# Kernel optimization log

Hardware: AMD Instinct MI355X
Metric: run time of the kernel (lower is better)

Reference implementation:

```python
import jax, jax.numpy as jnp
import numpy as np

NUM_ROUTES = 32 * 6 * 6  # 1152
NUM_CAPS = 10
IN_DIM = 8
OUT_DIM = 16
NUM_ITERS = 3

def _conv(x, w, stride):
    return jax.lax.conv_general_dilated(
        x, w, window_strides=(stride, stride), padding='VALID',
        dimension_numbers=('NCHW', 'OIHW', 'NCHW'))

def _squash(u):
    # squash over last axis, exactly as torch code (no eps)
    sn = (u ** 2).sum(-1, keepdims=True)
    return sn * u / ((1.0 + sn) * jnp.sqrt(sn))

def setup_inputs() -> dict:
    key = jax.random.key(0)
    ks = jax.random.split(key, 10)
    B = 512
    data = jax.random.normal(ks[0], (B, 1, 28, 28), dtype=jnp.float32)
    conv_w = jax.random.normal(ks[1], (256, 1, 9, 9), dtype=jnp.float32) * 0.05
    conv_b = jnp.zeros((256,), dtype=jnp.float32)
    # 8 primary-capsule convs stacked caps-major -> fused conv [8*32,256,9,9]
    pc_w = jax.random.normal(ks[2], (8 * 32, 256, 9, 9), dtype=jnp.float32) * 0.01
    pc_b = jnp.zeros((8 * 32,), dtype=jnp.float32)
    W = jax.random.normal(ks[3], (NUM_ROUTES, NUM_CAPS, OUT_DIM, IN_DIM), dtype=jnp.float32)
    enc_w1 = jax.random.normal(ks[4], (512, OUT_DIM * NUM_CAPS), dtype=jnp.float32) * 0.05
    enc_b1 = jnp.zeros((512,), dtype=jnp.float32)
    enc_w2 = jax.random.normal(ks[5], (9, 512), dtype=jnp.float32) * 0.05
    enc_b2 = jnp.zeros((9,), dtype=jnp.float32)
    return dict(data=data, conv_w=conv_w, conv_b=conv_b, pc_w=pc_w, pc_b=pc_b,
                W=W, enc_w1=enc_w1, enc_b1=enc_b1, enc_w2=enc_w2, enc_b2=enc_b2)

def reference(data, conv_w, conv_b, pc_w, pc_b, W, enc_w1, enc_b1, enc_w2, enc_b2):
    B = data.shape[0]
    # ConvLayer: conv + relu -> [B,256,20,20]
    x = jax.nn.relu(_conv(data, conv_w, 1) + conv_b[None, :, None, None])
    # PrimaryCaps: 8 stride-2 convs (fused, caps-major channels) -> [B,256,6,6]
    u = _conv(x, pc_w, 2) + pc_b[None, :, None, None]
    # torch: stack(dim=1) then view(B, num_routes, -1) == reshape caps-major flat
    u = u.reshape(B, NUM_ROUTES, IN_DIM)
    u = _squash(u)  # [B,R,8]
    # WaferCaps: u_hat[b,r,c,o] = sum_i W[r,c,o,i] * u[b,r,i]
    u_hat = jnp.einsum('rcoi,bri->brco', W, u)  # [B,R,C,O]
    b_ij = jnp.zeros((NUM_ROUTES, NUM_CAPS), dtype=u_hat.dtype)
    v = None
    for it in range(NUM_ITERS):
        c_ij = jax.nn.softmax(b_ij, axis=0)  # softmax over routes (dim=1 in torch)
        s = jnp.einsum('rc,brco->bco', c_ij, u_hat)  # [B,C,O]
        # original squashes [B,1,C,O,1] over last (size-1) dim -> elementwise
        s2 = s ** 2
        v = s2 * s / ((1.0 + s2) * jnp.sqrt(s2))  # = s*|s|/(1+s^2)
        if it < NUM_ITERS - 1:
            a = jnp.einsum('brco,bco->brc', u_hat, v)  # [B,R,C]
            b_ij = b_ij + a.mean(axis=0)
    # Encoder: flatten [B,C,O] row-major -> [B,160]
    flat = v.reshape(B, NUM_CAPS * OUT_DIM)
    h = jax.nn.relu(flat @ enc_w1.T + enc_b1)  # dropout is identity at eval
    out = jax.nn.sigmoid(h @ enc_w2.T + enc_b2)
    return out
```

## Files before the change

kernel.cpp:

```cpp
#include <hip/hip_runtime.h>
#include <hip/hip_bf16.h>
#include <stdint.h>


typedef __bf16 bf16_t;
typedef __bf16 bf16x4 __attribute__((ext_vector_type(4)));
typedef __bf16 bf16x8 __attribute__((ext_vector_type(8)));
typedef float f32x4 __attribute__((ext_vector_type(4)));
typedef int i32x4 __attribute__((ext_vector_type(4)));
typedef int i32x8 __attribute__((ext_vector_type(8)));

__device__ __forceinline__ void gload_lds16(const void* g, void* l) {
    __builtin_amdgcn_global_load_lds((const __attribute__((address_space(1))) void*)g,
                                     (__attribute__((address_space(3))) void*)l, 16, 0, 0);
}

#define MEMBAR() asm volatile("" ::: "memory")
#define HW_BARRIER() do { MEMBAR(); __builtin_amdgcn_s_barrier(); MEMBAR(); } while (0)

__device__ __forceinline__ uint8_t fp8b(float v) {
    return (uint8_t)(__builtin_amdgcn_cvt_pk_fp8_f32(v, 0.f, 0, false) & 0xFF);
}

__global__ void k_init_bij(float* bij) {
    int i = blockIdx.x * 256 + threadIdx.x;
    if (i < 1152 * 10) bij[i] = 0.f;
}

__global__ void k_w1t(const float* __restrict__ w1, float* __restrict__ w1t) {
    int i = blockIdx.x * 256 + threadIdx.x;
    int j = i / 160, k = i % 160;
    w1t[k * 512 + j] = w1[i];
}

__global__ void k_w1c(const float* __restrict__ cw, bf16_t* __restrict__ Bc1) {
    int idx = blockIdx.x * 256 + threadIdx.x;
    if (idx >= 26624) return;
    int oc = idx / 104, k = idx % 104;
    Bc1[idx] = (k < 81) ? (bf16_t)cw[oc * 81 + k] : (bf16_t)0.f;
}

__global__ __launch_bounds__(256) void k_w2t(const float* __restrict__ pcw,
                                             uint8_t* __restrict__ w2t8) {
    __shared__ uint16_t tmp16[10368];
    int oc = blockIdx.x, tid = threadIdx.x;
    const float* src = pcw + (size_t)oc * 20736;
    for (int q2 = tid; q2 < 10368; q2 += 256) {
        float a = src[q2 * 2] * 64.f;
        float b = src[q2 * 2 + 1] * 64.f;
        uint32_t pk = __builtin_amdgcn_cvt_pk_fp8_f32(a, b, 0, false);
        tmp16[q2] = (uint16_t)(pk & 0xFFFF);
    }
    __syncthreads();
    uint32_t* dst = (uint32_t*)(w2t8 + (size_t)oc * 20736);
    for (int w = tid; w < 5184; w += 256) {
        int k = w * 4;
        int t = k >> 8, ic0 = k & 255;
        uint32_t r = 0;
#pragma unroll
        for (int j = 0; j < 4; ++j) {
            int s = (ic0 + j) * 81 + t;
            uint32_t b = (tmp16[s >> 1] >> ((s & 1) * 8)) & 0xFF;
            r |= b << (8 * j);
        }
        dst[w] = r;
    }
}

__global__ __launch_bounds__(256) void k_im2col(const float* __restrict__ data,
                                                bf16_t* __restrict__ Acol) {
    __shared__ float img[784];
    int b = blockIdx.x, tid = threadIdx.x;
    for (int i = tid; i < 784; i += 256) img[i] = data[b * 784 + i];
    __syncthreads();
    for (int c = tid; c < 5200; c += 256) {
        int pos = c / 13, kc = c % 13;
        int oh = pos / 20, ow = pos % 20;
        bf16x8 v;
#pragma unroll
        for (int j = 0; j < 8; ++j) {
            int k = kc * 8 + j;
            float x = 0.f;
            if (k < 81) {
                int kh = k / 9, kw = k % 9;
                x = img[(oh + kh) * 28 + ow + kw];
            }
            v[j] = (bf16_t)x;
        }
        *(bf16x8*)&Acol[((size_t)b * 400 + pos) * 104 + kc * 8] = v;
    }
}

__global__ __launch_bounds__(512) void k_c1gemm(const bf16_t* __restrict__ Acol,
                                                const bf16_t* __restrict__ Bc1,
                                                const float* __restrict__ cb,
                                                uint8_t* __restrict__ xt8) {
    __shared__ __align__(16) bf16_t As[128 * 104];
    __shared__ __align__(16) bf16_t Bs[256 * 104];
    int tid = threadIdx.x, lane = tid & 63, wave = tid >> 6;
    int wm = wave >> 2, wn = wave & 3;
    for (int i = tid; i < 3328; i += 512) {
        int byte = i * 16;
        int r = byte / 208;
        int c16 = (byte - r * 208) >> 4;
        gload_lds16(Bc1 + r * 104 + c16 * 8, (char*)Bs + byte);
    }
    int mr = wm * 64 + (lane & 15);
    int nr = wn * 64 + (lane & 15);
    float bias[4];
#pragma unroll
    for (int nj = 0; nj < 4; ++nj) bias[nj] = cb[nr + nj * 16];

    for (int t = 0; t < 2; ++t) {
        int m0 = (blockIdx.x + t * 800) * 128;
        for (int i = tid; i < 1664; i += 512) {
            int byte = i * 16;
            int r = byte / 208;
            int c16 = (byte - r * 208) >> 4;
            gload_lds16(Acol + (size_t)(m0 + r) * 104 + c16 * 8, (char*)As + byte);
        }
        asm volatile("s_waitcnt vmcnt(0)" ::: "memory");
        HW_BARRIER();
        f32x4 acc[4][4];
#pragma unroll
        for (int mi = 0; mi < 4; ++mi)
#pragma unroll
            for (int nj = 0; nj < 4; ++nj) acc[mi][nj] = (f32x4){0.f, 0.f, 0.f, 0.f};
#pragma unroll
        for (int kk = 0; kk < 3; ++kk) {
            int ch = (kk * 4 + (lane >> 4)) * 8;
            bf16x8 af[4], bfr[4];
#pragma unroll
            for (int i = 0; i < 4; ++i) af[i] = *(const bf16x8*)&As[(mr + i * 16) * 104 + ch];
#pragma unroll
            for (int j = 0; j < 4; ++j) bfr[j] = *(const bf16x8*)&Bs[(nr + j * 16) * 104 + ch];
#pragma unroll
            for (int mi = 0; mi < 4; ++mi)
#pragma unroll
                for (int nj = 0; nj < 4; ++nj)
                    acc[mi][nj] = __builtin_amdgcn_mfma_f32_16x16x32_bf16(af[mi], bfr[nj], acc[mi][nj], 0, 0, 0);
        }
        int mbase = m0 + wm * 64 + (lane >> 4) * 4;
#pragma unroll
        for (int mi = 0; mi < 4; ++mi)
#pragma unroll
            for (int nj = 0; nj < 4; ++nj)
#pragma unroll
                for (int j = 0; j < 4; ++j)
                    xt8[(size_t)(mbase + mi * 16 + j) * 256 + nr + nj * 16] =
                        fp8b(fmaxf(acc[mi][nj][j] + bias[nj], 0.f));
        HW_BARRIER();
    }
}

__global__ __launch_bounds__(256) void k_pcgemm(const uint8_t* __restrict__ xt8,
                                                const uint8_t* __restrict__ w2t8,
                                                bf16_t* __restrict__ parts) {
    __shared__ __align__(16) uint8_t As[128 * 128];
    __shared__ __align__(16) uint8_t Bs[128 * 128];
    int bid = blockIdx.x;
    int mt = bid % 144;
    int nt = (bid / 144) & 1;
    int ks = bid / 288;
    int m0 = mt * 128, n0 = nt * 128;
    int tid = threadIdx.x, lane = tid & 63, wave = tid >> 6;

    int csrc = (tid & 7) ^ ((tid >> 3) & 7);
    int arow[4];
#pragma unroll
    for (int p = 0; p < 4; ++p) {
        int m = m0 + p * 32 + (tid >> 3);
        int bb = m / 36, pos = m % 36;
        int oh = pos / 6, ow = pos % 6;
        arow[p] = ((bb * 20 + oh * 2) * 20 + ow * 2) * 256;
    }
    const uint8_t* bbase = w2t8 + (size_t)(n0 + (tid >> 3)) * 20736 + csrc * 16;

    f32x4 acc[4][4];
#pragma unroll
    for (int mi = 0; mi < 4; ++mi)
#pragma unroll
        for (int ni = 0; ni < 4; ++ni) acc[mi][ni] = (f32x4){0.f, 0.f, 0.f, 0.f};

    int g0 = ks * 81;
    int mr = (wave >> 1) * 64 + (lane & 15);
    int nr = (wave & 1) * 64 + (lane & 15);
    int rx = lane & 7;
    int c0 = (2 * (lane >> 4)) ^ rx;
    int c1 = (2 * (lane >> 4) + 1) ^ rx;

    for (int it = 0; it < 81; ++it) {
        int g = g0 + it;
        int t = g >> 1, icb = g & 1;
        int kh = t / 9, kw = t - (t / 9) * 9;
        int aoff = (kh * 20 + kw) * 256 + icb * 128 + csrc * 16;
#pragma unroll
        for (int p = 0; p < 4; ++p) {
            gload_lds16(xt8 + arow[p] + aoff, &As[p * 4096 + tid * 16]);
            gload_lds16(bbase + (size_t)p * 32 * 20736 + (size_t)g * 128, &Bs[p * 4096 + tid * 16]);
        }
        __syncthreads();
        i32x8 af[4], bfr[4];
#pragma unroll
        for (int i = 0; i < 4; ++i) {
            i32x4 lo = *(const i32x4*)&As[(mr + i * 16) * 128 + c0 * 16];
            i32x4 hi = *(const i32x4*)&As[(mr + i * 16) * 128 + c1 * 16];
            af[i][0] = lo[0]; af[i][1] = lo[1]; af[i][2] = lo[2]; af[i][3] = lo[3];
            af[i][4] = hi[0]; af[i][5] = hi[1]; af[i][6] = hi[2]; af[i][7] = hi[3];
        }
#pragma unroll
        for (int i = 0; i < 4; ++i) {
            i32x4 lo = *(const i32x4*)&Bs[(nr + i * 16) * 128 + c0 * 16];
            i32x4 hi = *(const i32x4*)&Bs[(nr + i * 16) * 128 + c1 * 16];
            bfr[i][0] = lo[0]; bfr[i][1] = lo[1]; bfr[i][2] = lo[2]; bfr[i][3] = lo[3];
            bfr[i][4] = hi[0]; bfr[i][5] = hi[1]; bfr[i][6] = hi[2]; bfr[i][7] = hi[3];
        }
#pragma unroll
        for (int mi = 0; mi < 4; ++mi)
#pragma unroll
            for (int ni = 0; ni < 4; ++ni)
                acc[mi][ni] = __builtin_amdgcn_mfma_scale_f32_16x16x128_f8f6f4(
                    af[mi], bfr[ni], acc[mi][ni], 0, 0, 0, 0x7F7F7F7F, 0, 0x79797979);
        __syncthreads();
    }

    bf16_t* out = parts + (size_t)ks * 4718592;
    int mbase = m0 + (wave >> 1) * 64 + (lane >> 4) * 4;
    int nbase = n0 + (wave & 1) * 64 + (lane & 15);
#pragma unroll
    for (int mi = 0; mi < 4; ++mi)
#pragma unroll
        for (int ni = 0; ni < 4; ++ni)
#pragma unroll
            for (int j = 0; j < 4; ++j)
                out[(size_t)(mbase + mi * 16 + j) * 256 + nbase + ni * 16] = (bf16_t)acc[mi][ni][j];
}

__global__ __launch_bounds__(256) void k_squash(const bf16_t* __restrict__ parts,
                                                const float* __restrict__ pcb,
                                                bf16_t* __restrict__ ub) {
    __shared__ float s[36 * 257];
    int b = blockIdx.x, tid = threadIdx.x;
    for (int i = tid; i < 9216; i += 256) {
        float a = pcb[i & 255];
#pragma unroll
        for (int p = 0; p < 2; ++p) a += (float)parts[(size_t)p * 4718592 + (size_t)b * 9216 + i];
        s[(i >> 8) * 257 + (i & 255)] = a;
    }
    __syncthreads();
    for (int r = tid; r < 1152; r += 256) {
        int flat0 = r * 8;
        float val[8], sn = 0.f;
#pragma unroll
        for (int e = 0; e < 8; ++e) {
            int f = flat0 + e;
            float x = s[(f % 36) * 257 + f / 36];
            val[e] = x;
            sn += x * x;
        }
        float scale = sn / ((1.f + sn) * sqrtf(sn));
        bf16x8 vv;
#pragma unroll
        for (int e = 0; e < 8; ++e) vv[e] = (bf16_t)(val[e] * scale);
        *(bf16x8*)&ub[(size_t)b * 9216 + flat0] = vv;
    }
}

__global__ __launch_bounds__(256) void k_uT(const bf16_t* __restrict__ ub, bf16_t* __restrict__ uT) {
    __shared__ bf16_t t[64 * 66];
    int kt = blockIdx.x % 144, bt = blockIdx.x / 144;
    int k0 = kt * 64, b0 = bt * 64;
    int tid = threadIdx.x;
    int c8 = tid & 7;
#pragma unroll
    for (int p = 0; p < 2; ++p) {
        int r = p * 32 + (tid >> 3);
        bf16x8 vv = *(const bf16x8*)&ub[(size_t)(b0 + r) * 9216 + k0 + c8 * 8];
        uint32_t u4[4];
        *(bf16x8*)u4 = vv;
#pragma unroll
        for (int j2 = 0; j2 < 4; ++j2)
            *(uint32_t*)&t[r * 66 + c8 * 8 + j2 * 2] = u4[j2];
    }
    __syncthreads();
#pragma unroll
    for (int p = 0; p < 2; ++p) {
        int kp = p * 32 + (tid >> 3);
        bf16x8 vv;
#pragma unroll
        for (int j = 0; j < 8; ++j) vv[j] = t[(c8 * 8 + j) * 66 + kp];
        *(bf16x8*)&uT[(size_t)(k0 + kp) * 512 + b0 + c8 * 8] = vv;
    }
}

__global__ __launch_bounds__(256) void k_fold(const float* __restrict__ bij,
                                              const float* __restrict__ W,
                                              bf16_t* __restrict__ cw2T) {
    __shared__ float red[256];
    int idx0 = blockIdx.x * 256;
    int co = idx0 / 9216;
    int c = co >> 4, o = co & 15;
    int tid = threadIdx.x;
    float mx = -1e30f;
    for (int r = tid; r < 1152; r += 256) mx = fmaxf(mx, bij[r * 10 + c]);
    red[tid] = mx; __syncthreads();
    for (int s = 128; s > 0; s >>= 1) { if (tid < s) red[tid] = fmaxf(red[tid], red[tid + s]); __syncthreads(); }
    float mxv = red[0];
    __syncthreads();
    float sm = 0.f;
    for (int r = tid; r < 1152; r += 256) sm += expf(bij[r * 10 + c] - mxv);
    red[tid] = sm; __syncthreads();
    for (int s = 128; s > 0; s >>= 1) { if (tid < s) red[tid] += red[tid + s]; __syncthreads(); }
    float inv = 1.f / red[0];
    int k = (idx0 + tid) % 9216;
    int r = k >> 3, i = k & 7;
    float cij = expf(bij[r * 10 + c] - mxv) * inv;
    cw2T[idx0 + tid] = (bf16_t)(cij * W[((size_t)(r * 10 + c) * 16 + o) * 8 + i]);
}

__global__ __launch_bounds__(256) void k_rgemm(const bf16_t* __restrict__ A,
                                               const bf16_t* __restrict__ B,
                                               float* __restrict__ Cp,
                                               int Kfull, int steps, int mtiles) {
    __shared__ __align__(16) bf16_t As[64 * 64];
    __shared__ __align__(16) bf16_t Bs[160 * 64];
    int bid = blockIdx.x;
    int mt = bid % mtiles, ks = bid / mtiles;
    int m0 = mt * 64;
    int k0 = ks * steps * 64;
    int tid = threadIdx.x, lane = tid & 63, wave = tid >> 6;
    int srow = tid >> 3;
    int csrc = (tid & 7) ^ (srow & 7);
    const bf16_t* asrc[2];
    const bf16_t* bsrc[5];
#pragma unroll
    for (int p = 0; p < 2; ++p)
        asrc[p] = A + (size_t)(m0 + p * 32 + srow) * Kfull + k0 + csrc * 8;
#pragma unroll
    for (int p = 0; p < 5; ++p)
        bsrc[p] = B + (size_t)(p * 32 + srow) * Kfull + k0 + csrc * 8;

    f32x4 acc[2][5];
#pragma unroll
    for (int mi = 0; mi < 2; ++mi)
#pragma unroll
        for (int nj = 0; nj < 5; ++nj) acc[mi][nj] = (f32x4){0.f, 0.f, 0.f, 0.f};

    int mr = (wave >> 1) * 32 + (lane & 15);
    int nr = (wave & 1) * 80 + (lane & 15);
    int rx = lane & 7;

    for (int it = 0; it < steps; ++it) {
#pragma unroll
        for (int p = 0; p < 2; ++p) gload_lds16(asrc[p] + it * 64, As + p * 2048 + tid * 8);
#pragma unroll
        for (int p = 0; p < 5; ++p) gload_lds16(bsrc[p] + it * 64, Bs + p * 2048 + tid * 8);
        __syncthreads();
#pragma unroll
        for (int kk = 0; kk < 2; ++kk) {
            int ch = ((kk * 4 + (lane >> 4)) ^ rx) * 8;
            bf16x8 af[2], bfr[5];
#pragma unroll
            for (int i = 0; i < 2; ++i) af[i] = *(const bf16x8*)&As[(mr + i * 16) * 64 + ch];
#pragma unroll
            for (int j = 0; j < 5; ++j) bfr[j] = *(const bf16x8*)&Bs[(nr + j * 16) * 64 + ch];
#pragma unroll
            for (int mi = 0; mi < 2; ++mi)
#pragma unroll
                for (int nj = 0; nj < 5; ++nj)
                    acc[mi][nj] = __builtin_amdgcn_mfma_f32_16x16x32_bf16(af[mi], bfr[nj], acc[mi][nj], 0, 0, 0);
        }
        __syncthreads();
    }

    float* out = Cp + (size_t)ks * ((size_t)mtiles * 64 * 160);
    int mbase = m0 + (wave >> 1) * 32 + (lane >> 4) * 4;
    int nbase = (wave & 1) * 80 + (lane & 15);
#pragma unroll
    for (int mi = 0; mi < 2; ++mi)
#pragma unroll
        for (int nj = 0; nj < 5; ++nj)
#pragma unroll
            for (int j = 0; j < 4; ++j)
                out[(size_t)(mbase + mi * 16 + j) * 160 + nbase + nj * 16] = acc[mi][nj][j];
}

__global__ void k_vcomp(const float* __restrict__ sp, float* __restrict__ v,
                        bf16_t* __restrict__ vT) {
    int idx = blockIdx.x * 256 + threadIdx.x;
    float s = 0.f;
#pragma unroll
    for (int p = 0; p < 36; ++p) s += sp[(size_t)p * 81920 + idx];
    float val = s * fabsf(s) / (1.f + s * s);
    v[idx] = val;
    int b = idx / 160, co = idx % 160;
    vT[(size_t)co * 512 + b] = (bf16_t)val;
}

__global__ __launch_bounds__(256) void k_ggemm2(const bf16_t* __restrict__ uT,
                                                const bf16_t* __restrict__ vT,
                                                const float* __restrict__ W,
                                                float* __restrict__ bij) {
    __shared__ __align__(16) bf16_t As[64 * 64];
    __shared__ __align__(16) bf16_t Bs[160 * 64];
    __shared__ float Gl[64 * 161];
    int mt = blockIdx.x;
    int m0 = mt * 64;
    int tid = threadIdx.x, lane = tid & 63, wave = tid >> 6;
    int srow = tid >> 3;
    int csrc = (tid & 7) ^ (srow & 7);
    const bf16_t* asrc[2];
    const bf16_t* bsrc[5];
#pragma unroll
    for (int p = 0; p < 2; ++p)
        asrc[p] = uT + (size_t)(m0 + p * 32 + srow) * 512 + csrc * 8;
#pragma unroll
    for (int p = 0; p < 5; ++p)
        bsrc[p] = vT + (size_t)(p * 32 + srow) * 512 + csrc * 8;

    f32x4 acc[2][5];
#pragma unroll
    for (int mi = 0; mi < 2; ++mi)
#pragma unroll
        for (int nj = 0; nj < 5; ++nj) acc[mi][nj] = (f32x4){0.f, 0.f, 0.f, 0.f};

    int mr = (wave >> 1) * 32 + (lane & 15);
    int nr = (wave & 1) * 80 + (lane & 15);
    int rx = lane & 7;

    for (int it = 0; it < 8; ++it) {
#pragma unroll
        for (int p = 0; p < 2; ++p) gload_lds16(asrc[p] + it * 64, As + p * 2048 + tid * 8);
#pragma unroll
        for (int p = 0; p < 5; ++p) gload_lds16(bsrc[p] + it * 64, Bs + p * 2048 + tid * 8);
        __syncthreads();
#pragma unroll
        for (int kk = 0; kk < 2; ++kk) {
            int ch = ((kk * 4 + (lane >> 4)) ^ rx) * 8;
            bf16x8 af[2], bfr[5];
#pragma unroll
            for (int i = 0; i < 2; ++i) af[i] = *(const bf16x8*)&As[(mr + i * 16) * 64 + ch];
#pragma unroll
            for (int j = 0; j < 5; ++j) bfr[j] = *(const bf16x8*)&Bs[(nr + j * 16) * 64 + ch];
#pragma unroll
            for (int mi = 0; mi < 2; ++mi)
#pragma unroll
                for (int nj = 0; nj < 5; ++nj)
                    acc[mi][nj] = __builtin_amdgcn_mfma_f32_16x16x32_bf16(af[mi], bfr[nj], acc[mi][nj], 0, 0, 0);
        }
        __syncthreads();
    }

    int mbl = (wave >> 1) * 32 + (lane >> 4) * 4;
    int nbase = (wave & 1) * 80 + (lane & 15);
#pragma unroll
    for (int mi = 0; mi < 2; ++mi)
#pragma unroll
        for (int nj = 0; nj < 5; ++nj)
#pragma unroll
            for (int j = 0; j < 4; ++j)
                Gl[(mbl + mi * 16 + j) * 161 + nbase + nj * 16] = acc[mi][nj][j] * (1.0f / 512.0f);
    __syncthreads();
    if (tid < 80) {
        int rl = tid / 10, c = tid % 10;
        int r = mt * 8 + rl;
        const float* wbase = W + (size_t)(r * 10 + c) * 128;
        float s = 0.f;
#pragma unroll
        for (int o = 0; o < 16; ++o)
#pragma unroll
            for (int i = 0; i < 8; ++i)
                s += wbase[o * 8 + i] * Gl[(rl * 8 + i) * 161 + c * 16 + o];
        bij[r * 10 + c] += s;
    }
}

__global__ __launch_bounds__(256) void k_enc(const float* __restrict__ v,
                                             const float* __restrict__ w1t,
                                             const float* __restrict__ b1,
                                             const float* __restrict__ w2,
                                             const float* __restrict__ b2,
                                             float* __restrict__ out) {
    __shared__ float fl[160];
    __shared__ float h[512];
    int b = blockIdx.x, tid = threadIdx.x;
    if (tid < 160) fl[tid] = v[b * 160 + tid];
    __syncthreads();
    for (int j = tid; j < 512; j += 256) {
        float s = b1[j];
#pragma unroll 8
        for (int k = 0; k < 160; ++k) s += fl[k] * w1t[k * 512 + j];
        h[j] = fmaxf(s, 0.f);
    }
    __syncthreads();
    int wave = tid >> 6, lane = tid & 63;
    for (int j = wave; j < 9; j += 4) {
        float p = 0.f;
#pragma unroll
        for (int l = lane; l < 512; l += 64) p += h[l] * w2[j * 512 + l];
#pragma unroll
        for (int off = 32; off > 0; off >>= 1) p += __shfl_down(p, off, 64);
        if (lane == 0) out[b * 9 + j] = 1.f / (1.f + expf(-(p + b2[j])));
    }
}

extern "C" void kernel_launch(void* const* d_in, const int* in_sizes, int n_in,
                              void* d_out, int out_size, void* d_ws, size_t ws_size,
                              hipStream_t stream) {
    const float* data   = (const float*)d_in[0];
    const float* conv_w = (const float*)d_in[1];
    const float* conv_b = (const float*)d_in[2];
    const float* pc_w   = (const float*)d_in[3];
    const float* pc_b   = (const float*)d_in[4];
    const float* W      = (const float*)d_in[5];
    const float* enc_w1 = (const float*)d_in[6];
    const float* enc_b1 = (const float*)d_in[7];
    const float* enc_w2 = (const float*)d_in[8];
    const float* enc_b2 = (const float*)d_in[9];

    char* ws = (char*)d_ws;
    uint8_t* xt8   = (uint8_t*)(ws + 0);
    uint8_t* w2t8  = (uint8_t*)(ws + 52428800);
    bf16_t*  parts = (bf16_t*)(ws + 57737216);
    bf16_t*  Acol  = (bf16_t*)(ws + 76611584);
    bf16_t*  uT    = (bf16_t*)(ws + 76611584);
    bf16_t*  cw2T  = (bf16_t*)(ws + 86048768);
    float*   sp    = (float*)(ws + 88997888);
    bf16_t*  ub    = (bf16_t*)(ws + 119209984);
    float*   v     = (float*)(ws + 128647168);
    bf16_t*  vT    = (bf16_t*)(ws + 128974848);
    float*   w1t   = (float*)(ws + 129138688);
    float*   bij   = (float*)(ws + 129466368);
    bf16_t*  Bc1   = (bf16_t*)(ws + 129512448);
    float*   outp  = (float*)d_out;

    hipLaunchKernelGGL(k_init_bij, dim3(45), dim3(256), 0, stream, bij);
    hipLaunchKernelGGL(k_w1t, dim3(320), dim3(256), 0, stream, enc_w1, w1t);
    hipLaunchKernelGGL(k_w1c, dim3(104), dim3(256), 0, stream, conv_w, Bc1);
    hipLaunchKernelGGL(k_w2t, dim3(256), dim3(256), 0, stream, pc_w, w2t8);
    hipLaunchKernelGGL(k_im2col, dim3(512), dim3(256), 0, stream, data, Acol);
    hipLaunchKernelGGL(k_c1gemm, dim3(800), dim3(512), 0, stream, Acol, Bc1, conv_b, xt8);
    hipLaunchKernelGGL(k_pcgemm, dim3(576), dim3(256), 0, stream, xt8, w2t8, parts);
    hipLaunchKernelGGL(k_squash, dim3(512), dim3(256), 0, stream, parts, pc_b, ub);
    hipLaunchKernelGGL(k_uT, dim3(1152), dim3(256), 0, stream, ub, uT);
    for (int it = 0; it < 3; ++it) {
        hipLaunchKernelGGL(k_fold, dim3(5760), dim3(256), 0, stream, bij, W, cw2T);
        hipLaunchKernelGGL(k_rgemm, dim3(288), dim3(256), 0, stream, ub, cw2T, sp, 9216, 4, 8);
        hipLaunchKernelGGL(k_vcomp, dim3(320), dim3(256), 0, stream, sp, v, vT);
        if (it < 2) {
            hipLaunchKernelGGL(k_ggemm2, dim3(144), dim3(256), 0, stream, uT, vT, W, bij);
        }
    }
    hipLaunchKernelGGL(k_enc, dim3(512), dim3(256), 0, stream, v, w1t, enc_b1, enc_w2, enc_b2, outp);
}
```

Before: 331.3 us.

## Fuse prep kernels, inline im2col into conv1 GEMM, split pcgemm K three ways, bf16 partials

Merges the three small weight-prep and init kernels into one launch, and builds the conv1 im2col tile directly in LDS inside the GEMM so the Acol buffer is never written or read. The primary-capsule GEMM K dimension is split into three slices instead of two, giving more blocks, and the squash kernel now sums three partials. Routing GEMM partial sums are stored as bf16 instead of fp32, halving that traffic. The costs are LDS-side im2col arithmetic in the conv GEMM, an extra partial pass, and lower-precision accumulation of the route partials.

```diff
diff --git a/kernel.cpp b/kernel.cpp
--- a/kernel.cpp
+++ b/kernel.cpp
@@ -16,28 +16,29 @@
 }
 
 #define MEMBAR() asm volatile("" ::: "memory")
-#define HW_BARRIER() do { MEMBAR(); __builtin_amdgcn_s_barrier(); MEMBAR(); } while (0)
 
 __device__ __forceinline__ uint8_t fp8b(float v) {
     return (uint8_t)(__builtin_amdgcn_cvt_pk_fp8_f32(v, 0.f, 0, false) & 0xFF);
 }
 
-__global__ void k_init_bij(float* bij) {
-    int i = blockIdx.x * 256 + threadIdx.x;
-    if (i < 1152 * 10) bij[i] = 0.f;
-}
-
-__global__ void k_w1t(const float* __restrict__ w1, float* __restrict__ w1t) {
-    int i = blockIdx.x * 256 + threadIdx.x;
-    int j = i / 160, k = i % 160;
-    w1t[k * 512 + j] = w1[i];
-}
-
-__global__ void k_w1c(const float* __restrict__ cw, bf16_t* __restrict__ Bc1) {
-    int idx = blockIdx.x * 256 + threadIdx.x;
-    if (idx >= 26624) return;
-    int oc = idx / 104, k = idx % 104;
-    Bc1[idx] = (k < 81) ? (bf16_t)cw[oc * 81 + k] : (bf16_t)0.f;
+__global__ void k_prep(const float* __restrict__ w1, const float* __restrict__ cw,
+                       float* __restrict__ w1t, bf16_t* __restrict__ Bc1,
+                       float* __restrict__ bij) {
+    int blk = blockIdx.x, tid = threadIdx.x;
+    if (blk < 45) {
+        int i = blk * 256 + tid;
+        if (i < 11520) bij[i] = 0.f;
+    } else if (blk < 365) {
+        int i = (blk - 45) * 256 + tid;
+        int j = i / 160, k = i % 160;
+        w1t[k * 512 + j] = w1[i];
+    } else {
+        int i = (blk - 365) * 256 + tid;
+        if (i < 26624) {
+            int oc = i / 104, k = i % 104;
+            Bc1[i] = (k < 81) ? (bf16_t)cw[oc * 81 + k] : (bf16_t)0.f;
+        }
+    }
 }
 
 __global__ __launch_bounds__(256) void k_w2t(const float* __restrict__ pcw,
@@ -67,36 +68,13 @@
     }
 }
 
-__global__ __launch_bounds__(256) void k_im2col(const float* __restrict__ data,
-                                                bf16_t* __restrict__ Acol) {
-    __shared__ float img[784];
-    int b = blockIdx.x, tid = threadIdx.x;
-    for (int i = tid; i < 784; i += 256) img[i] = data[b * 784 + i];
-    __syncthreads();
-    for (int c = tid; c < 5200; c += 256) {
-        int pos = c / 13, kc = c % 13;
-        int oh = pos / 20, ow = pos % 20;
-        bf16x8 v;
-#pragma unroll
-        for (int j = 0; j < 8; ++j) {
-            int k = kc * 8 + j;
-            float x = 0.f;
-            if (k < 81) {
-                int kh = k / 9, kw = k % 9;
-                x = img[(oh + kh) * 28 + ow + kw];
-            }
-            v[j] = (bf16_t)x;
-        }
-        *(bf16x8*)&Acol[((size_t)b * 400 + pos) * 104 + kc * 8] = v;
-    }
-}
-
-__global__ __launch_bounds__(512) void k_c1gemm(const bf16_t* __restrict__ Acol,
+__global__ __launch_bounds__(512) void k_c1gemm(const float* __restrict__ data,
                                                 const bf16_t* __restrict__ Bc1,
                                                 const float* __restrict__ cb,
                                                 uint8_t* __restrict__ xt8) {
     __shared__ __align__(16) bf16_t As[128 * 104];
     __shared__ __align__(16) bf16_t Bs[256 * 104];
+    __shared__ float img[1568];
     int tid = threadIdx.x, lane = tid & 63, wave = tid >> 6;
     int wm = wave >> 2, wn = wave & 3;
     for (int i = tid; i < 3328; i += 512) {
@@ -113,14 +91,27 @@
 
     for (int t = 0; t < 2; ++t) {
         int m0 = (blockIdx.x + t * 800) * 128;
-        for (int i = tid; i < 1664; i += 512) {
-            int byte = i * 16;
-            int r = byte / 208;
-            int c16 = (byte - r * 208) >> 4;
-            gload_lds16(Acol + (size_t)(m0 + r) * 104 + c16 * 8, (char*)As + byte);
+        int bfirst = m0 / 400;
+        int blast = (m0 + 127) / 400;
+        int nimg = blast - bfirst + 1;
+        __syncthreads();
+        for (int i = tid; i < nimg * 784; i += 512)
+            img[i] = data[(size_t)bfirst * 784 + i];
+        __syncthreads();
+        for (int e = tid; e < 13312; e += 512) {
+            int r = e / 104, k = e - r * 104;
+            int m = m0 + r;
+            int b = m / 400, pos = m - b * 400;
+            int oh = pos / 20, ow = pos - oh * 20;
+            float x = 0.f;
+            if (k < 81) {
+                int kh = k / 9, kw = k - kh * 9;
+                x = img[(b - bfirst) * 784 + (oh + kh) * 28 + ow + kw];
+            }
+            As[e] = (bf16_t)x;
         }
         asm volatile("s_waitcnt vmcnt(0)" ::: "memory");
-        HW_BARRIER();
+        __syncthreads();
         f32x4 acc[4][4];
 #pragma unroll
         for (int mi = 0; mi < 4; ++mi)
@@ -149,7 +140,6 @@
                 for (int j = 0; j < 4; ++j)
                     xt8[(size_t)(mbase + mi * 16 + j) * 256 + nr + nj * 16] =
                         fp8b(fmaxf(acc[mi][nj][j] + bias[nj], 0.f));
-        HW_BARRIER();
     }
 }
 
@@ -182,14 +172,14 @@
 #pragma unroll
         for (int ni = 0; ni < 4; ++ni) acc[mi][ni] = (f32x4){0.f, 0.f, 0.f, 0.f};
 
-    int g0 = ks * 81;
+    int g0 = ks * 54;
     int mr = (wave >> 1) * 64 + (lane & 15);
     int nr = (wave & 1) * 64 + (lane & 15);
     int rx = lane & 7;
     int c0 = (2 * (lane >> 4)) ^ rx;
     int c1 = (2 * (lane >> 4) + 1) ^ rx;
 
-    for (int it = 0; it < 81; ++it) {
+    for (int it = 0; it < 54; ++it) {
         int g = g0 + it;
         int t = g >> 1, icb = g & 1;
         int kh = t / 9, kw = t - (t / 9) * 9;
@@ -244,7 +234,7 @@
     for (int i = tid; i < 9216; i += 256) {
         float a = pcb[i & 255];
 #pragma unroll
-        for (int p = 0; p < 2; ++p) a += (float)parts[(size_t)p * 4718592 + (size_t)b * 9216 + i];
+        for (int p = 0; p < 3; ++p) a += (float)parts[(size_t)p * 4718592 + (size_t)b * 9216 + i];
         s[(i >> 8) * 257 + (i & 255)] = a;
     }
     __syncthreads();
@@ -320,7 +310,7 @@
 
 __global__ __launch_bounds__(256) void k_rgemm(const bf16_t* __restrict__ A,
                                                const bf16_t* __restrict__ B,
-                                               float* __restrict__ Cp,
+                                               bf16_t* __restrict__ Cp,
                                                int Kfull, int steps, int mtiles) {
     __shared__ __align__(16) bf16_t As[64 * 64];
     __shared__ __align__(16) bf16_t Bs[160 * 64];
@@ -373,7 +363,7 @@
         __syncthreads();
     }
 
-    float* out = Cp + (size_t)ks * ((size_t)mtiles * 64 * 160);
+    bf16_t* out = Cp + (size_t)ks * ((size_t)mtiles * 64 * 160);
     int mbase = m0 + (wave >> 1) * 32 + (lane >> 4) * 4;
     int nbase = (wave & 1) * 80 + (lane & 15);
 #pragma unroll
@@ -382,15 +372,15 @@
         for (int nj = 0; nj < 5; ++nj)
 #pragma unroll
             for (int j = 0; j < 4; ++j)
-                out[(size_t)(mbase + mi * 16 + j) * 160 + nbase + nj * 16] = acc[mi][nj][j];
-}
-
-__global__ void k_vcomp(const float* __restrict__ sp, float* __restrict__ v,
+                out[(size_t)(mbase + mi * 16 + j) * 160 + nbase + nj * 16] = (bf16_t)acc[mi][nj][j];
+}
+
+__global__ void k_vcomp(const bf16_t* __restrict__ sp, float* __restrict__ v,
                         bf16_t* __restrict__ vT) {
     int idx = blockIdx.x * 256 + threadIdx.x;
     float s = 0.f;
 #pragma unroll
-    for (int p = 0; p < 36; ++p) s += sp[(size_t)p * 81920 + idx];
+    for (int p = 0; p < 36; ++p) s += (float)sp[(size_t)p * 81920 + idx];
     float val = s * fabsf(s) / (1.f + s * s);
     v[idx] = val;
     int b = idx / 160, co = idx % 160;
@@ -522,25 +512,21 @@
     uint8_t* xt8   = (uint8_t*)(ws + 0);
     uint8_t* w2t8  = (uint8_t*)(ws + 52428800);
     bf16_t*  parts = (bf16_t*)(ws + 57737216);
-    bf16_t*  Acol  = (bf16_t*)(ws + 76611584);
-    bf16_t*  uT    = (bf16_t*)(ws + 76611584);
-    bf16_t*  cw2T  = (bf16_t*)(ws + 86048768);
-    float*   sp    = (float*)(ws + 88997888);
-    bf16_t*  ub    = (bf16_t*)(ws + 119209984);
-    float*   v     = (float*)(ws + 128647168);
-    bf16_t*  vT    = (bf16_t*)(ws + 128974848);
-    float*   w1t   = (float*)(ws + 129138688);
-    float*   bij   = (float*)(ws + 129466368);
-    bf16_t*  Bc1   = (bf16_t*)(ws + 129512448);
+    bf16_t*  uT    = (bf16_t*)(ws + 86048768);
+    bf16_t*  cw2T  = (bf16_t*)(ws + 95485952);
+    bf16_t*  sp    = (bf16_t*)(ws + 98435072);
+    bf16_t*  ub    = (bf16_t*)(ws + 104333312);
+    float*   v     = (float*)(ws + 113770496);
+    bf16_t*  vT    = (bf16_t*)(ws + 114098176);
+    float*   w1t   = (float*)(ws + 114262016);
+    float*   bij   = (float*)(ws + 114589696);
+    bf16_t*  Bc1   = (bf16_t*)(ws + 114635776);
     float*   outp  = (float*)d_out;
 
-    hipLaunchKernelGGL(k_init_bij, dim3(45), dim3(256), 0, stream, bij);
-    hipLaunchKernelGGL(k_w1t, dim3(320), dim3(256), 0, stream, enc_w1, w1t);
-    hipLaunchKernelGGL(k_w1c, dim3(104), dim3(256), 0, stream, conv_w, Bc1);
+    hipLaunchKernelGGL(k_prep, dim3(469), dim3(256), 0, stream, enc_w1, conv_w, w1t, Bc1, bij);
     hipLaunchKernelGGL(k_w2t, dim3(256), dim3(256), 0, stream, pc_w, w2t8);
-    hipLaunchKernelGGL(k_im2col, dim3(512), dim3(256), 0, stream, data, Acol);
-    hipLaunchKernelGGL(k_c1gemm, dim3(800), dim3(512), 0, stream, Acol, Bc1, conv_b, xt8);
-    hipLaunchKernelGGL(k_pcgemm, dim3(576), dim3(256), 0, stream, xt8, w2t8, parts);
+    hipLaunchKernelGGL(k_c1gemm, dim3(800), dim3(512), 0, stream, data, Bc1, conv_b, xt8);
+    hipLaunchKernelGGL(k_pcgemm, dim3(864), dim3(256), 0, stream, xt8, w2t8, parts);
     hipLaunchKernelGGL(k_squash, dim3(512), dim3(256), 0, stream, parts, pc_b, ub);
     hipLaunchKernelGGL(k_uT, dim3(1152), dim3(256), 0, stream, ub, uT);
     for (int it = 0; it < 3; ++it) {
```

After: 353.6 us. 1.07x slower.
